# Kernel tuning notes

Measured on AMD Instinct MI355X. Metric: run time of the kernel, lower is better.

Reference implementation:

```python
import jax, jax.numpy as jnp
import numpy as np

H, W = 200, 200            # image_size
X_RANGE = (0.0, 100.0)
Y_RANGE = (0.0, 100.0)
SIZE = 36                   # kernel 'size' from source
SIGMA = 3.0
K = SIZE + 1                # kernel is 37x37 (arange(-18, 19))


def _gaussian_kernel():
    r = jnp.arange(-(SIZE // 2), SIZE // 2 + 1, dtype=jnp.float32)
    k1 = jnp.exp(-(r ** 2) / (2.0 * SIGMA ** 2))
    k2 = k1[:, None] * k1[None, :]
    return k2 / k2.sum()    # [K, K]


def setup_inputs() -> dict:
    key = jax.random.key(0)
    # trajectory coords in world units [0, 100) -> spread over whole map
    x_t = jax.random.uniform(key, (512, 64, 2), dtype=jnp.float32) * 100.0
    return {"x_t": x_t}


def reference(x_t):
    B, T, _ = x_t.shape
    x_scale = W / (X_RANGE[1] - X_RANGE[0])
    y_scale = H / (Y_RANGE[1] - Y_RANGE[0])
    # .long() in torch truncates toward zero; inputs are >= 0 here so astype(int32) matches
    x_pix = ((x_t[:, :, 0] - X_RANGE[0]) * x_scale).astype(jnp.int32)   # [B, T]
    y_pix = H - ((x_t[:, :, 1] - Y_RANGE[0]) * y_scale).astype(jnp.int32)
    valid = ~(jnp.isnan(x_t[:, :, 0]) | jnp.isnan(x_t[:, :, 1]))        # [B, T]

    half = SIZE // 2
    x_start = jnp.clip(x_pix - half, 0, W - SIZE)
    y_start = jnp.clip(y_pix - half, 0, H - SIZE)
    x_end = jnp.clip(x_pix + half, 0, W)
    y_end = jnp.clip(y_pix + half, 0, H)
    kx = x_end - x_start    # patch width  (<= 36, kernel[:,:kx] = top-left slice)
    ky = y_end - y_start    # patch height

    kern = _gaussian_kernel()                       # [K, K]
    r = jnp.arange(K)
    c = jnp.arange(K)
    # mask: kernel[:ky, :kx] slice, and point validity            [B, T, K, K]
    mask = ((r[None, None, :, None] < ky[..., None, None])
            & (c[None, None, None, :] < kx[..., None, None])
            & valid[..., None, None])
    vals = jnp.where(mask, kern[None, None, :, :], 0.0)            # [B, T, K, K]
    rows = jnp.clip(y_start[..., None, None] + r[None, None, :, None], 0, H - 1)
    cols = jnp.clip(x_start[..., None, None] + c[None, None, None, :], 0, W - 1)
    rows = jnp.broadcast_to(rows, (B, T, K, K))
    cols = jnp.broadcast_to(cols, (B, T, K, K))
    flat = (rows * W + cols).reshape(B, -1)                        # [B, T*K*K]

    # parallel scatter-add splat of all Gaussian patches
    heat = jnp.zeros((B, H * W), jnp.float32)
    heat = heat.at[jnp.arange(B)[:, None], flat].add(vals.reshape(B, -1))
    heat = heat.reshape(B, H, W)

    # per-image max normalization (max over dim1 then dim2 == max over both)
    m = heat.max(axis=(1, 2), keepdims=True)
    return heat / (m + 1e-10)
```

## Files before the change

### kernel.cpp

```cpp
#include <hip/hip_runtime.h>


#define NT 64
#define TDIM 224
#define NTL 7
#define BLK 1024

typedef short bf16x8 __attribute__((ext_vector_type(8)));
typedef float f32x16 __attribute__((ext_vector_type(16)));

static __device__ inline unsigned short f2bf(float f) {
    unsigned int u = __float_as_uint(f);
    u = (u + 0x7FFFu + ((u >> 16) & 1u)) >> 16;
    return (unsigned short)u;
}

struct __align__(16) SMem {
    unsigned short Rm[TDIM][64];
    unsigned short Cm[TDIM][64];
    float k1f[37];
    float wmax[14];
};

__global__ __launch_bounds__(BLK) void heatmap_kernel(const float* __restrict__ x_t,
                                                      float* __restrict__ out) {
    __shared__ SMem s;
    const int tid  = threadIdx.x;
    const int lane = tid & 63;
    const int wv   = tid >> 6;
    const int b    = blockIdx.x;

    {
        uint4 z = {0u, 0u, 0u, 0u};
        uint4* base = (uint4*)s.Rm;
        #pragma unroll
        for (int i = 0; i < 4; ++i) {
            const int idx = tid + BLK * i;
            if (idx < 3584) base[idx] = z;
        }
    }
    if (tid < 37) {
        float sum = 0.0f, mine = 0.0f;
        #pragma unroll
        for (int i = 0; i < 37; ++i) {
            float r = (float)(i - 18);
            float v = expf(-(r * r) * (1.0f / 18.0f));
            sum += v;
            if (i == tid) mine = v;
        }
        s.k1f[tid] = mine / sum;
    }
    __syncthreads();

    {
        const int p   = (tid >> 3) & 63;
        const int isC = tid >> 9;
        const int j   = tid & 7;
        const float2 xy = *(const float2*)(x_t + (size_t)b * 128 + 2 * p);
        const bool valid = (xy.x == xy.x) && (xy.y == xy.y);
        const int xp = (int)(xy.x * 2.0f);
        const int yp = 200 - (int)(xy.y * 2.0f);
        const int xs = min(max(xp - 18, 0), 164);
        const int ys = min(max(yp - 18, 0), 164);
        const int kx = valid ? (min(max(xp + 18, 0), 200) - xs) : 0;
        const int ky = valid ? (min(max(yp + 18, 0), 200) - ys) : 0;
        const int start = isC ? xs : ys;
        const int len   = isC ? kx : ky;
        char* dst = isC ? (char*)s.Cm : (char*)s.Rm;
        #pragma unroll
        for (int i = 0; i < 5; ++i) {
            const int rel = j * 5 + i;
            if (rel < len) {
                const int row = start + rel;
                const int off = (2 * p) ^ ((row & 7) << 4);
                *(unsigned short*)(dst + row * 128 + off) = f2bf(s.k1f[rel]);
            }
        }
    }
    __syncthreads();

    const int swl  = (lane & 7) << 4;
    const int ty   = wv >> 1;
    const int half = wv & 1;
    const int tx0  = half ? 4 : 0;
    const int tx1  = half ? 7 : 4;

    bf16x8 A[4];
    if (ty < NTL) {
        const char* ab = (const char*)s.Rm + (ty * 32 + (lane & 31)) * 128;
        #pragma unroll
        for (int m = 0; m < 4; ++m)
            A[m] = *(const bf16x8*)(ab + ((16 * (2 * m + (lane >> 5))) ^ swl));
    }

    float gmax = 0.0f;
    if (ty < NTL) {
        for (int tx = tx0; tx < tx1; ++tx) {
            const char* bb = (const char*)s.Cm + (tx * 32 + (lane & 31)) * 128;
            f32x16 acc;
            #pragma unroll
            for (int r = 0; r < 16; ++r) acc[r] = 0.0f;
            #pragma unroll
            for (int m = 0; m < 4; ++m) {
                bf16x8 B = *(const bf16x8*)(bb + ((16 * (2 * m + (lane >> 5))) ^ swl));
                acc = __builtin_amdgcn_mfma_f32_32x32x16_bf16(A[m], B, acc, 0, 0, 0);
            }
            #pragma unroll
            for (int r = 0; r < 16; ++r) gmax = fmaxf(gmax, acc[r]);
        }
    }
    #pragma unroll
    for (int off = 32; off > 0; off >>= 1) gmax = fmaxf(gmax, __shfl_xor(gmax, off));
    if (ty < NTL && lane == 0) s.wmax[wv] = gmax;
    __syncthreads();
    float mm = s.wmax[0];
    #pragma unroll
    for (int w = 1; w < 14; ++w) mm = fmaxf(mm, s.wmax[w]);
    const float scale = 1.0f / (mm + 1e-10f);

    if (ty < NTL) {
        float* ob = out + (size_t)b * (200 * 200);
        const int colbase = lane & 31;
        const int rowoff  = ty * 32 + 4 * (lane >> 5);
        for (int tx = tx0; tx < tx1; ++tx) {
            const char* bb = (const char*)s.Cm + (tx * 32 + (lane & 31)) * 128;
            f32x16 acc;
            #pragma unroll
            for (int r = 0; r < 16; ++r) acc[r] = 0.0f;
            #pragma unroll
            for (int m = 0; m < 4; ++m) {
                bf16x8 B = *(const bf16x8*)(bb + ((16 * (2 * m + (lane >> 5))) ^ swl));
                acc = __builtin_amdgcn_mfma_f32_32x32x16_bf16(A[m], B, acc, 0, 0, 0);
            }
            const int gcol = tx * 32 + colbase;
            #pragma unroll
            for (int r = 0; r < 16; ++r) {
                int grow = rowoff + (r & 3) + 8 * (r >> 2);
                if (grow < 200 && gcol < 200)
                    ob[(size_t)grow * 200 + gcol] = acc[r] * scale;
            }
        }
    }
}

extern "C" void kernel_launch(void* const* d_in, const int* in_sizes, int n_in,
                              void* d_out, int out_size, void* d_ws, size_t ws_size,
                              hipStream_t stream) {
    const float* x_t = (const float*)d_in[0];
    float* out = (float*)d_out;
    const int B = in_sizes[0] / (NT * 2);
    heatmap_kernel<<<B, BLK, 0, stream>>>(x_t, out);
}
```

Before: 25.53 us.

## Switch to 16x16 MFMA tiles held in registers and process two images per block

Replaces the 32x32x16 MFMA tiling with 16x16x32 tiles so each wave keeps a full 16-row strip of the heatmap (13 accumulators) in registers. The matmul is therefore computed once instead of being recomputed for the max pass and the store pass. Blocks shrink to 896 threads and each handles two images in a loop, with launch bounds for higher occupancy. The trade-offs are higher register pressure and narrower 16-column store segments.

```diff
diff --git a/kernel.cpp b/kernel.cpp
--- a/kernel.cpp
+++ b/kernel.cpp
@@ -3,11 +3,10 @@
 
 #define NT 64
 #define TDIM 224
-#define NTL 7
-#define BLK 1024
+#define BLK 896
 
 typedef short bf16x8 __attribute__((ext_vector_type(8)));
-typedef float f32x16 __attribute__((ext_vector_type(16)));
+typedef float f32x4  __attribute__((ext_vector_type(4)));
 
 static __device__ inline unsigned short f2bf(float f) {
     unsigned int u = __float_as_uint(f);
@@ -22,23 +21,14 @@
     float wmax[14];
 };
 
-__global__ __launch_bounds__(BLK) void heatmap_kernel(const float* __restrict__ x_t,
-                                                      float* __restrict__ out) {
+__global__ __launch_bounds__(BLK, 4) void heatmap_kernel(const float* __restrict__ x_t,
+                                                         float* __restrict__ out) {
     __shared__ SMem s;
     const int tid  = threadIdx.x;
     const int lane = tid & 63;
     const int wv   = tid >> 6;
-    const int b    = blockIdx.x;
+    const int swl  = (lane & 7) << 4;
 
-    {
-        uint4 z = {0u, 0u, 0u, 0u};
-        uint4* base = (uint4*)s.Rm;
-        #pragma unroll
-        for (int i = 0; i < 4; ++i) {
-            const int idx = tid + BLK * i;
-            if (idx < 3584) base[idx] = z;
-        }
-    }
     if (tid < 37) {
         float sum = 0.0f, mine = 0.0f;
         #pragma unroll
@@ -50,94 +40,97 @@
         }
         s.k1f[tid] = mine / sum;
     }
-    __syncthreads();
 
-    {
-        const int p   = (tid >> 3) & 63;
-        const int isC = tid >> 9;
-        const int j   = tid & 7;
-        const float2 xy = *(const float2*)(x_t + (size_t)b * 128 + 2 * p);
-        const bool valid = (xy.x == xy.x) && (xy.y == xy.y);
-        const int xp = (int)(xy.x * 2.0f);
-        const int yp = 200 - (int)(xy.y * 2.0f);
-        const int xs = min(max(xp - 18, 0), 164);
-        const int ys = min(max(yp - 18, 0), 164);
-        const int kx = valid ? (min(max(xp + 18, 0), 200) - xs) : 0;
-        const int ky = valid ? (min(max(yp + 18, 0), 200) - ys) : 0;
-        const int start = isC ? xs : ys;
-        const int len   = isC ? kx : ky;
-        char* dst = isC ? (char*)s.Cm : (char*)s.Rm;
-        #pragma unroll
-        for (int i = 0; i < 5; ++i) {
-            const int rel = j * 5 + i;
-            if (rel < len) {
-                const int row = start + rel;
-                const int off = (2 * p) ^ ((row & 7) << 4);
-                *(unsigned short*)(dst + row * 128 + off) = f2bf(s.k1f[rel]);
+    for (int img = 0; img < 2; ++img) {
+        const int b = 2 * blockIdx.x + img;
+
+        __syncthreads();
+        {
+            uint4 z = {0u, 0u, 0u, 0u};
+            uint4* base = (uint4*)s.Rm;
+            #pragma unroll
+            for (int i = 0; i < 4; ++i) base[tid + BLK * i] = z;
+        }
+        __syncthreads();
+
+        {
+            const int isC = tid >= 448;
+            const int t2  = tid - (isC ? 448 : 0);
+            const int p   = t2 / 7;
+            const int j   = t2 - 7 * p;
+            const float2 xy = *(const float2*)(x_t + (size_t)b * 128 + 2 * p);
+            const bool valid = (xy.x == xy.x) && (xy.y == xy.y);
+            const int xp = (int)(xy.x * 2.0f);
+            const int yp = 200 - (int)(xy.y * 2.0f);
+            const int xs = min(max(xp - 18, 0), 164);
+            const int ys = min(max(yp - 18, 0), 164);
+            const int kx = valid ? (min(max(xp + 18, 0), 200) - xs) : 0;
+            const int ky = valid ? (min(max(yp + 18, 0), 200) - ys) : 0;
+            const int start = isC ? xs : ys;
+            const int len   = isC ? kx : ky;
+            char* dst = isC ? (char*)s.Cm : (char*)s.Rm;
+            #pragma unroll
+            for (int i = 0; i < 6; ++i) {
+                const int rel = j * 6 + i;
+                if (rel < len) {
+                    const int row = start + rel;
+                    const int off = (2 * p) ^ ((row & 7) << 4);
+                    *(unsigned short*)(dst + row * 128 + off) = f2bf(s.k1f[rel]);
+                }
             }
         }
-    }
-    __syncthreads();
+        __syncthreads();
 
-    const int swl  = (lane & 7) << 4;
-    const int ty   = wv >> 1;
-    const int half = wv & 1;
-    const int tx0  = half ? 4 : 0;
-    const int tx1  = half ? 7 : 4;
-
-    bf16x8 A[4];
-    if (ty < NTL) {
-        const char* ab = (const char*)s.Rm + (ty * 32 + (lane & 31)) * 128;
-        #pragma unroll
-        for (int m = 0; m < 4; ++m)
-            A[m] = *(const bf16x8*)(ab + ((16 * (2 * m + (lane >> 5))) ^ swl));
-    }
-
-    float gmax = 0.0f;
-    if (ty < NTL) {
-        for (int tx = tx0; tx < tx1; ++tx) {
-            const char* bb = (const char*)s.Cm + (tx * 32 + (lane & 31)) * 128;
-            f32x16 acc;
-            #pragma unroll
-            for (int r = 0; r < 16; ++r) acc[r] = 0.0f;
-            #pragma unroll
-            for (int m = 0; m < 4; ++m) {
-                bf16x8 B = *(const bf16x8*)(bb + ((16 * (2 * m + (lane >> 5))) ^ swl));
-                acc = __builtin_amdgcn_mfma_f32_32x32x16_bf16(A[m], B, acc, 0, 0, 0);
+        f32x4 acc[13];
+        float gmax = 0.0f;
+        if (wv < 13) {
+            bf16x8 A0, A1;
+            {
+                const char* ab = (const char*)s.Rm + (16 * wv + (lane & 15)) * 128;
+                A0 = *(const bf16x8*)(ab + ((16 * (lane >> 4)) ^ swl));
+                A1 = *(const bf16x8*)(ab + ((16 * (lane >> 4) + 64) ^ swl));
             }
             #pragma unroll
-            for (int r = 0; r < 16; ++r) gmax = fmaxf(gmax, acc[r]);
+            for (int t = 0; t < 13; ++t) {
+                #pragma unroll
+                for (int r = 0; r < 4; ++r) acc[t][r] = 0.0f;
+            }
+            #pragma unroll
+            for (int t = 0; t < 13; ++t) {
+                const char* bb = (const char*)s.Cm + (16 * t + (lane & 15)) * 128;
+                bf16x8 B0 = *(const bf16x8*)(bb + ((16 * (lane >> 4)) ^ swl));
+                bf16x8 B1 = *(const bf16x8*)(bb + ((16 * (lane >> 4) + 64) ^ swl));
+                acc[t] = __builtin_amdgcn_mfma_f32_16x16x32_bf16(A0, B0, acc[t], 0, 0, 0);
+                acc[t] = __builtin_amdgcn_mfma_f32_16x16x32_bf16(A1, B1, acc[t], 0, 0, 0);
+            }
+            #pragma unroll
+            for (int t = 0; t < 13; ++t) {
+                #pragma unroll
+                for (int r = 0; r < 4; ++r) gmax = fmaxf(gmax, acc[t][r]);
+            }
         }
-    }
-    #pragma unroll
-    for (int off = 32; off > 0; off >>= 1) gmax = fmaxf(gmax, __shfl_xor(gmax, off));
-    if (ty < NTL && lane == 0) s.wmax[wv] = gmax;
-    __syncthreads();
-    float mm = s.wmax[0];
-    #pragma unroll
-    for (int w = 1; w < 14; ++w) mm = fmaxf(mm, s.wmax[w]);
-    const float scale = 1.0f / (mm + 1e-10f);
+        #pragma unroll
+        for (int off = 32; off > 0; off >>= 1) gmax = fmaxf(gmax, __shfl_xor(gmax, off));
+        if (lane == 0) s.wmax[wv] = gmax;
+        __syncthreads();
+        float mm = s.wmax[0];
+        #pragma unroll
+        for (int w = 1; w < 14; ++w) mm = fmaxf(mm, s.wmax[w]);
+        const float scale = 1.0f / (mm + 1e-10f);
 
-    if (ty < NTL) {
-        float* ob = out + (size_t)b * (200 * 200);
-        const int colbase = lane & 31;
-        const int rowoff  = ty * 32 + 4 * (lane >> 5);
-        for (int tx = tx0; tx < tx1; ++tx) {
-            const char* bb = (const char*)s.Cm + (tx * 32 + (lane & 31)) * 128;
-            f32x16 acc;
+        if (wv < 13) {
+            float* ob = out + (size_t)b * (200 * 200);
+            const int rbase = 16 * wv + 4 * (lane >> 4);
+            const int cbase = lane & 15;
             #pragma unroll
-            for (int r = 0; r < 16; ++r) acc[r] = 0.0f;
-            #pragma unroll
-            for (int m = 0; m < 4; ++m) {
-                bf16x8 B = *(const bf16x8*)(bb + ((16 * (2 * m + (lane >> 5))) ^ swl));
-                acc = __builtin_amdgcn_mfma_f32_32x32x16_bf16(A[m], B, acc, 0, 0, 0);
-            }
-            const int gcol = tx * 32 + colbase;
-            #pragma unroll
-            for (int r = 0; r < 16; ++r) {
-                int grow = rowoff + (r & 3) + 8 * (r >> 2);
-                if (grow < 200 && gcol < 200)
-                    ob[(size_t)grow * 200 + gcol] = acc[r] * scale;
+            for (int t = 0; t < 13; ++t) {
+                const int gcol = 16 * t + cbase;
+                #pragma unroll
+                for (int r = 0; r < 4; ++r) {
+                    const int grow = rbase + r;
+                    if (grow < 200 && gcol < 200)
+                        ob[(size_t)grow * 200 + gcol] = acc[t][r] * scale;
+                }
             }
         }
     }
@@ -149,5 +142,5 @@
     const float* x_t = (const float*)d_in[0];
     float* out = (float*)d_out;
     const int B = in_sizes[0] / (NT * 2);
-    heatmap_kernel<<<B, BLK, 0, stream>>>(x_t, out);
+    heatmap_kernel<<<B / 2, BLK, 0, stream>>>(x_t, out);
 }
```

Result: faster. 24.56 us (-3.8%).
